# Kernel optimization log

Hardware: AMD Instinct MI355X
Metric: run time of the kernel (lower is better)

## Reference

```python
import jax, jax.numpy as jnp
import numpy as np

HEADS = 16
DIM_HEAD = 64


def setup_inputs() -> dict:
    key = jax.random.key(0)
    k1, k2, k3, k4 = jax.random.split(key, 4)
    B, T, D = 4, 1024, 1024
    x = jax.random.normal(k1, (B, T, D), dtype=jnp.float32)
    w_qkv = jax.random.normal(k2, (3 * HEADS * DIM_HEAD, D), dtype=jnp.float32) * (1.0 / np.sqrt(D))
    w_out = jax.random.normal(k3, (D, HEADS * DIM_HEAD), dtype=jnp.float32) * (1.0 / np.sqrt(HEADS * DIM_HEAD))
    rel_bias = jax.random.normal(k4, (2 * 1024 - 1, HEADS), dtype=jnp.float32) * 0.02
    return {"x": x, "w_qkv": w_qkv, "w_out": w_out, "rel_bias": rel_bias}


def reference(x, w_qkv, w_out, rel_bias):
    b, t, _ = x.shape
    h, dh = HEADS, DIM_HEAD
    scale = dh ** (-0.5)
    qkv = x @ w_qkv.T  # [b, t, 3*h*dh]
    # einops 'b t (d k h) -> k b h t d': last axis factors as (dh, 3, h)
    qkv = qkv.reshape(b, t, dh, 3, h).transpose(3, 0, 4, 1, 2)  # [3, b, h, t, dh]
    q, k, v = qkv[0], qkv[1], qkv[2]
    scores = jnp.einsum('bhid,bhjd->bhij', q, k) * scale  # [b, h, t, t]
    # relative position bias: rel[i,j] = j - i + t - 1
    rel = jnp.arange(t)[None, :] - jnp.arange(t)[:, None] + (t - 1)  # [t, t]
    bias = rel_bias[rel]  # [t, t, h]
    scores = scores + bias.transpose(2, 0, 1)[None]  # [b, h, t, t]
    attn = jax.nn.softmax(scores, axis=-1)
    out = jnp.einsum('bhij,bhjd->bhid', attn, v)  # [b, h, t, dh]
    out = out.transpose(0, 2, 1, 3).reshape(b, t, h * dh)  # 'b h t d -> b t (h d)'
    return out @ w_out.T
```

## Files before the change

### kernel.cpp

```cpp
#include <hip/hip_runtime.h>
#include <hip/hip_bf16.h>

typedef short bf16x8 __attribute__((ext_vector_type(8)));
typedef float f32x4  __attribute__((ext_vector_type(4)));

typedef __attribute__((address_space(3))) void lds_t;
typedef __attribute__((address_space(1))) void gbl_t;

#define MFMA16(a,b,c) __builtin_amdgcn_mfma_f32_16x16x32_bf16((a),(b),(c),0,0,0)

__device__ __forceinline__ unsigned short f2bf(float f) {
    __hip_bfloat16 h = __float2bfloat16(f);
    return __builtin_bit_cast(unsigned short, h);
}
__device__ __forceinline__ float bf2f(unsigned short u) {
    __hip_bfloat16 h = __builtin_bit_cast(__hip_bfloat16, u);
    return __bfloat162float(h);
}

__global__ void prep_all(const float* __restrict__ x,
                         const float* __restrict__ w_qkv,
                         const float* __restrict__ w_out,
                         unsigned short* __restrict__ A1h,
                         unsigned short* __restrict__ W1h,
                         unsigned short* __restrict__ W3h) {
    const int NX = 4096 * 256, NW1 = 3072 * 256, NW3 = 1024 * 256;
    for (int idx = blockIdx.x * blockDim.x + threadIdx.x; idx < NX + NW1 + NW3;
         idx += gridDim.x * blockDim.x) {
        if (idx < NX) {
            int base = idx * 4;
            float4 v = *reinterpret_cast<const float4*>(x + base);
            ushort4 hi;
            hi.x = f2bf(v.x); hi.y = f2bf(v.y);
            hi.z = f2bf(v.z); hi.w = f2bf(v.w);
            *reinterpret_cast<ushort4*>(A1h + base) = hi;
        } else if (idx < NX + NW1) {
            int base = (idx - NX) * 4;
            int n = base >> 10, c = base & 1023;
            int d = n & 63, which = n >> 10, h = (n >> 6) & 15;
            int srow = d * 48 + which * 16 + h;
            float4 v =
                *reinterpret_cast<const float4*>(w_qkv + (size_t)srow * 1024 + c);
            ushort4 hi;
            hi.x = f2bf(v.x); hi.y = f2bf(v.y);
            hi.z = f2bf(v.z); hi.w = f2bf(v.w);
            *reinterpret_cast<ushort4*>(W1h + (size_t)n * 1024 + c) = hi;
        } else {
            int base = (idx - NX - NW1) * 4;
            float4 v = *reinterpret_cast<const float4*>(w_out + base);
            ushort4 hi;
            hi.x = f2bf(v.x); hi.y = f2bf(v.y);
            hi.z = f2bf(v.z); hi.w = f2bf(v.w);
            *reinterpret_cast<ushort4*>(W3h + base) = hi;
        }
    }
}

__global__ __launch_bounds__(512, 2) void gemm256_hi(
    const unsigned short* __restrict__ A, const unsigned short* __restrict__ B,
    unsigned short* __restrict__ outQ, unsigned short* __restrict__ outK,
    unsigned short* __restrict__ outV) {
    __shared__ unsigned short lds[65536];
    const int tid = threadIdx.x;
    const int wid = tid >> 6, lane = tid & 63;
    const int lrow = lane & 15, lgrp = lane >> 4;
    const int wr = wid >> 2, wc = wid & 3;
    const int mtile = blockIdx.y * 256, ntile = blockIdx.x * 256;

    const int csw = lgrp ^ ((lrow >> 1) & 3);
    const int aoff = (wr * 128 + lrow) * 32 + csw * 8;
    const int boff = 32768 + (wc * 64 + lrow) * 32 + csw * 8;

    const int sreg = wid * 2;
    const int srow0 = sreg * 16 + (lane >> 2);
    const int srow1 = (sreg + 1) * 16 + (lane >> 2);
    const int schunk = (lane & 3) ^ ((lane >> 3) & 3);
    const int sdst0 = sreg * 512;

    f32x4 acc[8][4];
#pragma unroll
    for (int i = 0; i < 8; ++i)
#pragma unroll
        for (int j = 0; j < 4; ++j) {
            f32x4 z = {0.f, 0.f, 0.f, 0.f};
            acc[i][j] = z;
        }

#pragma unroll
    for (int s0 = 0; s0 < 2; ++s0) {
        const int kb = s0 * 32;
        __builtin_amdgcn_global_load_lds(
            (const gbl_t*)(A + (size_t)(mtile + srow0) * 1024 + kb + schunk * 8),
            (lds_t*)(lds + s0 * 8192 + sdst0), 16, 0, 0);
        __builtin_amdgcn_global_load_lds(
            (const gbl_t*)(A + (size_t)(mtile + srow1) * 1024 + kb + schunk * 8),
            (lds_t*)(lds + s0 * 8192 + sdst0 + 512), 16, 0, 0);
        __builtin_amdgcn_global_load_lds(
            (const gbl_t*)(B + (size_t)(ntile + srow0) * 1024 + kb + schunk * 8),
            (lds_t*)(lds + 32768 + s0 * 8192 + sdst0), 16, 0, 0);
        __builtin_amdgcn_global_load_lds(
            (const gbl_t*)(B + (size_t)(ntile + srow1) * 1024 + kb + schunk * 8),
            (lds_t*)(lds + 32768 + s0 * 8192 + sdst0 + 512), 16, 0, 0);
    }
    asm volatile("s_waitcnt vmcnt(4)" ::: "memory");
    __syncthreads();

    for (int s = 0; s < 32; ++s) {
        const int sa = s & 3;
        const unsigned short* sbase = lds + sa * 8192;

        bf16x8 af[8];
#pragma unroll
        for (int i = 0; i < 8; ++i)
            af[i] = *reinterpret_cast<const bf16x8*>(sbase + aoff + i * 512);
        bf16x8 b0 = *reinterpret_cast<const bf16x8*>(sbase + boff);
        bf16x8 b1 = *reinterpret_cast<const bf16x8*>(sbase + boff + 512);

        if (s <= 29) {
            const int kb2 = (s + 2) * 32;
            const int s2 = (s + 2) & 3;
            __builtin_amdgcn_global_load_lds(
                (const gbl_t*)(A + (size_t)(mtile + srow0) * 1024 + kb2 + schunk * 8),
                (lds_t*)(lds + s2 * 8192 + sdst0), 16, 0, 0);
            __builtin_amdgcn_global_load_lds(
                (const gbl_t*)(A + (size_t)(mtile + srow1) * 1024 + kb2 + schunk * 8),
                (lds_t*)(lds + s2 * 8192 + sdst0 + 512), 16, 0, 0);
        }
        __builtin_amdgcn_s_setprio(1);
#pragma unroll
        for (int i = 0; i < 8; ++i) {
            acc[i][0] = MFMA16(af[i], b0, acc[i][0]);
            acc[i][1] = MFMA16(af[i], b1, acc[i][1]);
        }
        __builtin_amdgcn_s_setprio(0);

        bf16x8 b2 = *reinterpret_cast<const bf16x8*>(sbase + boff + 1024);
        bf16x8 b3 = *reinterpret_cast<const bf16x8*>(sbase + boff + 1536);
        if (s <= 29) {
            const int kb2 = (s + 2) * 32;
            const int s2 = (s + 2) & 3;
            __builtin_amdgcn_global_load_lds(
                (const gbl_t*)(B + (size_t)(ntile + srow0) * 1024 + kb2 + schunk * 8),
                (lds_t*)(lds + 32768 + s2 * 8192 + sdst0), 16, 0, 0);
            __builtin_amdgcn_global_load_lds(
                (const gbl_t*)(B + (size_t)(ntile + srow1) * 1024 + kb2 + schunk * 8),
                (lds_t*)(lds + 32768 + s2 * 8192 + sdst0 + 512), 16, 0, 0);
        }
        __builtin_amdgcn_s_setprio(1);
#pragma unroll
        for (int i = 0; i < 8; ++i) {
            acc[i][2] = MFMA16(af[i], b2, acc[i][2]);
            acc[i][3] = MFMA16(af[i], b3, acc[i][3]);
        }
        __builtin_amdgcn_s_setprio(0);

        if (s < 31) {
            if (s <= 29)
                asm volatile("s_waitcnt vmcnt(4)" ::: "memory");
            else
                asm volatile("s_waitcnt vmcnt(0)" ::: "memory");
            __syncthreads();
        }
    }

#pragma unroll
    for (int i = 0; i < 8; ++i) {
#pragma unroll
        for (int j = 0; j < 4; ++j) {
#pragma unroll
            for (int r = 0; r < 4; ++r) {
                float v = acc[i][j][r];
                int m = mtile + wr * 128 + i * 16 + lgrp * 4 + r;
                int n = ntile + wc * 64 + j * 16 + lrow;
                int which = n >> 10;
                int hh = (n >> 6) & 15;
                int d = n & 63;
                int b = m >> 10, t = m & 1023;
                unsigned short* dstp =
                    (which == 0) ? outQ : ((which == 1) ? outK : outV);
                dstp[((size_t)((b << 4) + hh) * 1024 + t) * 64 + d] = f2bf(v);
            }
        }
    }
}

__global__ __launch_bounds__(256, 3) void gemm_out_v4(
    const unsigned short* __restrict__ A, const unsigned short* __restrict__ B,
    float* __restrict__ outF) {
    __shared__ unsigned short As[4][64 * 32];
    __shared__ unsigned short Bs[4][128 * 32];
    const int tid = threadIdx.x;
    const int wid = tid >> 6, lane = tid & 63;
    const int lrow = lane & 15, lgrp = lane >> 4;
    const int wr = wid >> 1, wc = wid & 1;
    const int h = blockIdx.x;
    const int xcd = h & 7, within = h >> 3;
    const int mtile = (xcd * 8 + (within & 7)) * 64;
    const int ntile = (within >> 3) * 128;

    const int csw = lgrp ^ ((lrow >> 1) & 3);
    const int aoff = (wr * 32 + lrow) * 32 + csw * 8;
    const int boff = (wc * 64 + lrow) * 32 + csw * 8;

    const int srow = tid >> 2;
    const int schunk = (tid & 3) ^ ((tid >> 3) & 3);
    const unsigned short* Arow = A + (size_t)(mtile + srow) * 1024 + schunk * 8;
    const unsigned short* Brow0 = B + (size_t)(ntile + srow) * 1024 + schunk * 8;
    const unsigned short* Brow1 =
        B + (size_t)(ntile + 64 + srow) * 1024 + schunk * 8;

    f32x4 acc[2][4];
#pragma unroll
    for (int i = 0; i < 2; ++i)
#pragma unroll
        for (int j = 0; j < 4; ++j) {
            f32x4 z = {0.f, 0.f, 0.f, 0.f};
            acc[i][j] = z;
        }

#pragma unroll
    for (int s0 = 0; s0 < 2; ++s0) {
        const int kb = s0 * 32;
        __builtin_amdgcn_global_load_lds((const gbl_t*)(Arow + kb),
                                         (lds_t*)(&As[s0][0] + tid * 8), 16, 0,
                                         0);
        __builtin_amdgcn_global_load_lds((const gbl_t*)(Brow0 + kb),
                                         (lds_t*)(&Bs[s0][0] + tid * 8), 16, 0,
                                         0);
        __builtin_amdgcn_global_load_lds((const gbl_t*)(Brow1 + kb),
                                         (lds_t*)(&Bs[s0][0] + 2048 + tid * 8),
                                         16, 0, 0);
    }
    asm volatile("s_waitcnt vmcnt(3)" ::: "memory");
    __syncthreads();

    for (int s = 0; s < 32; ++s) {
        const int sa = s & 3;
        if (s <= 29) {
            const int kb = (s + 2) * 32;
            const int s2 = (s + 2) & 3;
            __builtin_amdgcn_global_load_lds((const gbl_t*)(Arow + kb),
                                             (lds_t*)(&As[s2][0] + tid * 8), 16,
                                             0, 0);
            __builtin_amdgcn_global_load_lds((const gbl_t*)(Brow0 + kb),
                                             (lds_t*)(&Bs[s2][0] + tid * 8), 16,
                                             0, 0);
            __builtin_amdgcn_global_load_lds(
                (const gbl_t*)(Brow1 + kb),
                (lds_t*)(&Bs[s2][0] + 2048 + tid * 8), 16, 0, 0);
        }
        bf16x8 af[2], bfv[4];
#pragma unroll
        for (int i = 0; i < 2; ++i)
            af[i] = *reinterpret_cast<const bf16x8*>(&As[sa][0] + aoff + i * 512);
#pragma unroll
        for (int j = 0; j < 4; ++j)
            bfv[j] =
                *reinterpret_cast<const bf16x8*>(&Bs[sa][0] + boff + j * 512);
        __builtin_amdgcn_s_setprio(1);
#pragma unroll
        for (int i = 0; i < 2; ++i)
#pragma unroll
            for (int j = 0; j < 4; ++j)
                acc[i][j] = MFMA16(af[i], bfv[j], acc[i][j]);
        __builtin_amdgcn_s_setprio(0);
        if (s < 31) {
            if (s <= 29)
                asm volatile("s_waitcnt vmcnt(3)" ::: "memory");
            else
                asm volatile("s_waitcnt vmcnt(0)" ::: "memory");
            __syncthreads();
        }
    }

#pragma unroll
    for (int i = 0; i < 2; ++i)
#pragma unroll
        for (int j = 0; j < 4; ++j)
#pragma unroll
            for (int r = 0; r < 4; ++r) {
                int m = mtile + wr * 32 + i * 16 + lgrp * 4 + r;
                int n = ntile + wc * 64 + j * 16 + lrow;
                outF[(size_t)m * 1024 + n] = acc[i][j][r];
            }
}

__global__ __launch_bounds__(256) void transpose_v(
    const unsigned short* __restrict__ Vb, unsigned short* __restrict__ Vtg) {
    __shared__ unsigned short L[64][72];
    const int tt = blockIdx.x, bh = blockIdx.y;
    const int tid = threadIdx.x;
#pragma unroll
    for (int e = 0; e < 2; ++e) {
        int chunk = e * 256 + tid;
        int r = chunk >> 3, c = (chunk & 7) * 8;
        uint4 v = *reinterpret_cast<const uint4*>(
            Vb + ((size_t)bh * 1024 + tt * 64 + r) * 64 + c);
        *reinterpret_cast<uint4*>(&L[r][c]) = v;
    }
    __syncthreads();
#pragma unroll
    for (int e = 0; e < 2; ++e) {
        int chunk = e * 256 + tid;
        int d = chunk >> 3, t0 = (chunk & 7) * 8;
        unsigned short tmp[8];
#pragma unroll
        for (int u = 0; u < 8; ++u) tmp[u] = L[t0 + u][d];
        *reinterpret_cast<uint4*>(Vtg + ((size_t)bh * 64 + d) * 1024 + tt * 64 +
                                  t0) = *reinterpret_cast<const uint4*>(tmp);
    }
}

__global__ __launch_bounds__(512) void attn_kernel(
    const unsigned short* __restrict__ Qb, const unsigned short* __restrict__ Kb,
    const unsigned short* __restrict__ Vtg, const float* __restrict__ rel_bias,
    unsigned short* __restrict__ A3) {
    const int qt = blockIdx.x;
    const int bh = blockIdx.y;
    const int b = bh >> 4, h = bh & 15;
    const int tid = threadIdx.x;
    const int w = tid >> 6, lane = tid & 63;
    const int lrow = lane & 15, lgrp = lane >> 4;
    const float LOG2E = 1.4426950408889634f;
    const float SCALE2 = 0.125f * 1.4426950408889634f;
    const float THR = 11.5f;

    __shared__ unsigned short Ks[2][64 * 64];
    __shared__ unsigned short Vs[2][64 * 64];
    __shared__ unsigned short Ps[8][16 * 64];
    __shared__ float Bias2[2][192];

    const unsigned short* Ktile = Kb + (size_t)bh * 1024 * 64;
    const unsigned short* Vtile = Vtg + (size_t)bh * 64 * 1024;

    const unsigned short* Qp =
        Qb + ((size_t)bh * 1024 + qt * 128 + w * 16 + lrow) * 64;
    bf16x8 qa0 = *reinterpret_cast<const bf16x8*>(Qp + lgrp * 8);
    bf16x8 qa1 = *reinterpret_cast<const bf16x8*>(Qp + 32 + lgrp * 8);

    const int sr0 = w * 8 + (lane >> 3);
    const int sc_lo = lane & 7;

    float m_run = -3.0e38f;
    float l_run = 0.f;
    f32x4 o_acc[4];
#pragma unroll
    for (int n = 0; n < 4; n++) {
        f32x4 z = {0.f, 0.f, 0.f, 0.f};
        o_acc[n] = z;
    }

    const int bbase = lgrp * 4 + 127 - w * 16 - lrow;

    {
        {
            int r = sr0;
            int c = sc_lo ^ (r & 7);
            __builtin_amdgcn_global_load_lds(
                (const gbl_t*)(Ktile + (size_t)r * 64 + c * 8),
                (lds_t*)(&Ks[0][0] + w * 512), 16, 0, 0);
            __builtin_amdgcn_global_load_lds(
                (const gbl_t*)(Vtile + (size_t)r * 1024 + c * 8),
                (lds_t*)(&Vs[0][0] + w * 512), 16, 0, 0);
        }
        if (tid < 192) {
            int rowi = 0 - qt * 128 + 896 + tid;
            rowi = (rowi < 2046) ? rowi : 2046;
            Bias2[0][tid] = rel_bias[(size_t)rowi * 16 + h] * LOG2E;
        }
        asm volatile("s_waitcnt vmcnt(0)" ::: "memory");
        __syncthreads();
    }

    for (int kv = 0; kv < 16; ++kv) {
        const int cur = kv & 1;
        if (kv < 15) {
            const int j0n = (kv + 1) * 64;
            int r = sr0;
            int c = sc_lo ^ (r & 7);
            __builtin_amdgcn_global_load_lds(
                (const gbl_t*)(Ktile + (size_t)(j0n + r) * 64 + c * 8),
                (lds_t*)(&Ks[cur ^ 1][0] + w * 512), 16, 0, 0);
            __builtin_amdgcn_global_load_lds(
                (const gbl_t*)(Vtile + (size_t)r * 1024 + j0n + c * 8),
                (lds_t*)(&Vs[cur ^ 1][0] + w * 512), 16, 0, 0);
            if (tid < 192) {
                int rowi = j0n - qt * 128 + 896 + tid;
                rowi = (rowi < 2046) ? rowi : 2046;
                Bias2[cur ^ 1][tid] = rel_bias[(size_t)rowi * 16 + h] * LOG2E;
            }
        }

        const unsigned short* kbuf = &Ks[cur][0];
        f32x4 s[4];
        __builtin_amdgcn_s_setprio(1);
#pragma unroll
        for (int f = 0; f < 4; ++f) {
            int krow = f * 16 + lrow;
            int sw0 = (lgrp ^ (lrow & 7)) * 8;
            int sw1 = ((4 | lgrp) ^ (lrow & 7)) * 8;
            bf16x8 kb0 = *reinterpret_cast<const bf16x8*>(kbuf + krow * 64 + sw0);
            bf16x8 kb1 = *reinterpret_cast<const bf16x8*>(kbuf + krow * 64 + sw1);
            f32x4 z = {0.f, 0.f, 0.f, 0.f};
            z = MFMA16(kb0, qa0, z);
            z = MFMA16(kb1, qa1, z);
            s[f] = z;
        }
        __builtin_amdgcn_s_setprio(0);

        float x[4][4];
        float pm = -3.0e38f;
#pragma unroll
        for (int f = 0; f < 4; ++f)
#pragma unroll
            for (int r = 0; r < 4; ++r) {
                float xv = s[f][r] * SCALE2 + Bias2[cur][bbase + f * 16 + r];
                x[f][r] = xv;
                pm = fmaxf(pm, xv);
            }
        pm = fmaxf(pm, __shfl_xor(pm, 16));
        pm = fmaxf(pm, __shfl_xor(pm, 32));

        if (!__all(pm - m_run <= THR)) {
            float mnew = fmaxf(m_run, pm);
            float corr = __builtin_amdgcn_exp2f(m_run - mnew);
            m_run = mnew;
            l_run *= corr;
            float cb[4];
#pragma unroll
            for (int r = 0; r < 4; ++r) cb[r] = __shfl(corr, lgrp * 4 + r);
#pragma unroll
            for (int n = 0; n < 4; n++)
#pragma unroll
                for (int r = 0; r < 4; r++) o_acc[n][r] *= cb[r];
        }

        float su = 0.f;
#pragma unroll
        for (int f = 0; f < 4; ++f)
#pragma unroll
            for (int r = 0; r < 4; ++r) {
                float pv = __builtin_amdgcn_exp2f(x[f][r] - m_run);
                x[f][r] = pv;
                su += pv;
            }
        l_run += su;

#pragma unroll
        for (int f = 0; f < 4; ++f) {
            unsigned int plo, phi;
            asm("v_cvt_pk_bf16_f32 %0, %1, %2"
                : "=v"(plo)
                : "v"(x[f][0]), "v"(x[f][1]));
            asm("v_cvt_pk_bf16_f32 %0, %1, %2"
                : "=v"(phi)
                : "v"(x[f][2]), "v"(x[f][3]));
            const int chunk = (f * 2 + (lgrp >> 1)) ^ (lrow & 7);
            uint2 pw;
            pw.x = plo;
            pw.y = phi;
            *reinterpret_cast<uint2*>(
                &Ps[w][lrow * 64 + chunk * 8 + (lgrp & 1) * 4]) = pw;
        }

        const unsigned short* vbuf = &Vs[cur][0];
        __builtin_amdgcn_s_setprio(1);
#pragma unroll
        for (int jc = 0; jc < 2; ++jc) {
            int pc = ((4 * jc + lgrp) ^ (lrow & 7)) * 8;
            bf16x8 pa =
                *reinterpret_cast<const bf16x8*>(&Ps[w][0] + lrow * 64 + pc);
#pragma unroll
            for (int n = 0; n < 4; n++) {
                int vrow = n * 16 + lrow;
                bf16x8 vb =
                    *reinterpret_cast<const bf16x8*>(vbuf + vrow * 64 + pc);
                o_acc[n] = MFMA16(pa, vb, o_acc[n]);
            }
        }
        __builtin_amdgcn_s_setprio(0);

        if (kv < 15) {
            asm volatile("s_waitcnt vmcnt(0)" ::: "memory");
            __syncthreads();
        }
    }

    float lt = l_run + __shfl_xor(l_run, 16);
    lt += __shfl_xor(lt, 32);
    float rl[4];
#pragma unroll
    for (int r = 0; r < 4; ++r) rl[r] = 1.0f / __shfl(lt, lgrp * 4 + r);

#pragma unroll
    for (int n = 0; n < 4; n++) {
#pragma unroll
        for (int r = 0; r < 4; r++) {
            float val = o_acc[n][r] * rl[r];
            int ia = qt * 128 + w * 16 + lgrp * 4 + r;
            size_t m = (size_t)b * 1024 + ia;
            int col = h * 64 + n * 16 + lrow;
            A3[m * 1024 + col] = f2bf(val);
        }
    }
}

extern "C" void kernel_launch(void* const* d_in, const int* in_sizes, int n_in,
                              void* d_out, int out_size, void* d_ws,
                              size_t ws_size, hipStream_t stream) {
    const float* x = (const float*)d_in[0];
    const float* w_qkv = (const float*)d_in[1];
    const float* w_out = (const float*)d_in[2];
    const float* rel_bias = (const float*)d_in[3];
    float* out = (float*)d_out;

    char* ws = (char*)d_ws;
    size_t off = 0;
    auto alloc = [&](size_t bytes) {
        char* p = ws + off;
        off += (bytes + 255) & ~(size_t)255;
        return p;
    };
    unsigned short* A1h = (unsigned short*)alloc((size_t)4096 * 1024 * 2);
    unsigned short* W1h = (unsigned short*)alloc((size_t)3072 * 1024 * 2);
    unsigned short* Qb = (unsigned short*)alloc((size_t)64 * 1024 * 64 * 2);
    unsigned short* Kb = (unsigned short*)alloc((size_t)64 * 1024 * 64 * 2);
    unsigned short* Vb = (unsigned short*)alloc((size_t)64 * 1024 * 64 * 2);
    unsigned short* A3h = (unsigned short*)alloc((size_t)4096 * 1024 * 2);
    unsigned short* W3h = (unsigned short*)alloc((size_t)1024 * 1024 * 2);
    unsigned short* Vtg = A1h;

    hipLaunchKernelGGL(prep_all, dim3(2048), dim3(256), 0, stream, x, w_qkv,
                       w_out, A1h, W1h, W3h);
    hipLaunchKernelGGL(gemm256_hi, dim3(12, 16), dim3(512), 0, stream, A1h, W1h,
                       Qb, Kb, Vb);
    hipLaunchKernelGGL(transpose_v, dim3(16, 64), dim3(256), 0, stream, Vb, Vtg);
    hipLaunchKernelGGL(attn_kernel, dim3(8, 64), dim3(512), 0, stream, Qb, Kb,
                       Vtg, rel_bias, A3h);
    hipLaunchKernelGGL(gemm_out_v4, dim3(512), dim3(256), 0, stream, A3h, W3h,
                       out);
}
```

Measured before the change: 108.6 us.

## Use 64-wide K double-buffered tiles in out-proj GEMM and preload full bias row

The output projection GEMM moves from a four-stage ring of 32-wide K slices to two buffers of 64-wide K slices. This halves the number of loop iterations and barriers, and its XOR swizzle now spans eight 16-byte chunks. The attention kernel loads the whole relative-bias window for the query tile into LDS once, so the per-iteration bias loads and their double-buffer slot are gone. The cost is a shallower prefetch in the GEMM, since each step now waits for vmcnt(0), and a larger bias LDS footprint that can reduce occupancy.

```diff
diff --git a/kernel.cpp b/kernel.cpp
--- a/kernel.cpp
+++ b/kernel.cpp
@@ -184,11 +184,11 @@
     }
 }
 
-__global__ __launch_bounds__(256, 3) void gemm_out_v4(
+__global__ __launch_bounds__(256, 3) void gemm_out_v5(
     const unsigned short* __restrict__ A, const unsigned short* __restrict__ B,
     float* __restrict__ outF) {
-    __shared__ unsigned short As[4][64 * 32];
-    __shared__ unsigned short Bs[4][128 * 32];
+    __shared__ unsigned short As[2][64 * 64];
+    __shared__ unsigned short Bs[2][128 * 64];
     const int tid = threadIdx.x;
     const int wid = tid >> 6, lane = tid & 63;
     const int lrow = lane & 15, lgrp = lane >> 4;
@@ -198,16 +198,15 @@
     const int mtile = (xcd * 8 + (within & 7)) * 64;
     const int ntile = (within >> 3) * 128;
 
-    const int csw = lgrp ^ ((lrow >> 1) & 3);
-    const int aoff = (wr * 32 + lrow) * 32 + csw * 8;
-    const int boff = (wc * 64 + lrow) * 32 + csw * 8;
-
-    const int srow = tid >> 2;
-    const int schunk = (tid & 3) ^ ((tid >> 3) & 3);
-    const unsigned short* Arow = A + (size_t)(mtile + srow) * 1024 + schunk * 8;
-    const unsigned short* Brow0 = B + (size_t)(ntile + srow) * 1024 + schunk * 8;
-    const unsigned short* Brow1 =
-        B + (size_t)(ntile + 64 + srow) * 1024 + schunk * 8;
+    const int srow = tid >> 3;
+    const int schunk = (tid & 7) ^ (srow & 7);
+    const unsigned short* Abase = A + (size_t)(mtile + srow) * 1024 + schunk * 8;
+    const unsigned short* Bbase = B + (size_t)(ntile + srow) * 1024 + schunk * 8;
+
+    const int csw0 = (lgrp ^ (lrow & 7)) * 8;
+    const int csw1 = ((4 | lgrp) ^ (lrow & 7)) * 8;
+    const int arow = wr * 32 + lrow;
+    const int brow = wc * 64 + lrow;
 
     f32x4 acc[2][4];
 #pragma unroll
@@ -219,56 +218,60 @@
         }
 
 #pragma unroll
-    for (int s0 = 0; s0 < 2; ++s0) {
-        const int kb = s0 * 32;
-        __builtin_amdgcn_global_load_lds((const gbl_t*)(Arow + kb),
-                                         (lds_t*)(&As[s0][0] + tid * 8), 16, 0,
-                                         0);
-        __builtin_amdgcn_global_load_lds((const gbl_t*)(Brow0 + kb),
-                                         (lds_t*)(&Bs[s0][0] + tid * 8), 16, 0,
-                                         0);
-        __builtin_amdgcn_global_load_lds((const gbl_t*)(Brow1 + kb),
-                                         (lds_t*)(&Bs[s0][0] + 2048 + tid * 8),
-                                         16, 0, 0);
-    }
-    asm volatile("s_waitcnt vmcnt(3)" ::: "memory");
+    for (int e = 0; e < 2; ++e)
+        __builtin_amdgcn_global_load_lds(
+            (const gbl_t*)(Abase + (size_t)e * 32 * 1024),
+            (lds_t*)(&As[0][0] + e * 2048 + tid * 8), 16, 0, 0);
+#pragma unroll
+    for (int e = 0; e < 4; ++e)
+        __builtin_amdgcn_global_load_lds(
+            (const gbl_t*)(Bbase + (size_t)e * 32 * 1024),
+            (lds_t*)(&Bs[0][0] + e * 2048 + tid * 8), 16, 0, 0);
+    asm volatile("s_waitcnt vmcnt(0)" ::: "memory");
     __syncthreads();
 
-    for (int s = 0; s < 32; ++s) {
-        const int sa = s & 3;
-        if (s <= 29) {
-            const int kb = (s + 2) * 32;
-            const int s2 = (s + 2) & 3;
-            __builtin_amdgcn_global_load_lds((const gbl_t*)(Arow + kb),
-                                             (lds_t*)(&As[s2][0] + tid * 8), 16,
-                                             0, 0);
-            __builtin_amdgcn_global_load_lds((const gbl_t*)(Brow0 + kb),
-                                             (lds_t*)(&Bs[s2][0] + tid * 8), 16,
-                                             0, 0);
-            __builtin_amdgcn_global_load_lds(
-                (const gbl_t*)(Brow1 + kb),
-                (lds_t*)(&Bs[s2][0] + 2048 + tid * 8), 16, 0, 0);
-        }
-        bf16x8 af[2], bfv[4];
+    for (int s = 0; s < 16; ++s) {
+        const int cur = s & 1;
+        if (s < 15) {
+            const int kb = (s + 1) * 64;
+            const int nx = cur ^ 1;
+#pragma unroll
+            for (int e = 0; e < 2; ++e)
+                __builtin_amdgcn_global_load_lds(
+                    (const gbl_t*)(Abase + (size_t)e * 32 * 1024 + kb),
+                    (lds_t*)(&As[nx][0] + e * 2048 + tid * 8), 16, 0, 0);
+#pragma unroll
+            for (int e = 0; e < 4; ++e)
+                __builtin_amdgcn_global_load_lds(
+                    (const gbl_t*)(Bbase + (size_t)e * 32 * 1024 + kb),
+                    (lds_t*)(&Bs[nx][0] + e * 2048 + tid * 8), 16, 0, 0);
+        }
+        bf16x8 a0[2], a1[2], b0[4], b1[4];
+#pragma unroll
+        for (int i = 0; i < 2; ++i) {
+            a0[i] = *reinterpret_cast<const bf16x8*>(&As[cur][0] +
+                                                     (arow + i * 16) * 64 + csw0);
+            a1[i] = *reinterpret_cast<const bf16x8*>(&As[cur][0] +
+                                                     (arow + i * 16) * 64 + csw1);
+        }
+#pragma unroll
+        for (int j = 0; j < 4; ++j) {
+            b0[j] = *reinterpret_cast<const bf16x8*>(&Bs[cur][0] +
+                                                     (brow + j * 16) * 64 + csw0);
+            b1[j] = *reinterpret_cast<const bf16x8*>(&Bs[cur][0] +
+                                                     (brow + j * 16) * 64 + csw1);
+        }
+        __builtin_amdgcn_s_setprio(1);
 #pragma unroll
         for (int i = 0; i < 2; ++i)
-            af[i] = *reinterpret_cast<const bf16x8*>(&As[sa][0] + aoff + i * 512);
-#pragma unroll
-        for (int j = 0; j < 4; ++j)
-            bfv[j] =
-                *reinterpret_cast<const bf16x8*>(&Bs[sa][0] + boff + j * 512);
-        __builtin_amdgcn_s_setprio(1);
-#pragma unroll
-        for (int i = 0; i < 2; ++i)
-#pragma unroll
-            for (int j = 0; j < 4; ++j)
-                acc[i][j] = MFMA16(af[i], bfv[j], acc[i][j]);
+#pragma unroll
+            for (int j = 0; j < 4; ++j) {
+                acc[i][j] = MFMA16(a0[i], b0[j], acc[i][j]);
+                acc[i][j] = MFMA16(a1[i], b1[j], acc[i][j]);
+            }
         __builtin_amdgcn_s_setprio(0);
-        if (s < 31) {
-            if (s <= 29)
-                asm volatile("s_waitcnt vmcnt(3)" ::: "memory");
-            else
-                asm volatile("s_waitcnt vmcnt(0)" ::: "memory");
+        if (s < 15) {
+            asm volatile("s_waitcnt vmcnt(0)" ::: "memory");
             __syncthreads();
         }
     }
@@ -328,7 +331,7 @@
     __shared__ unsigned short Ks[2][64 * 64];
     __shared__ unsigned short Vs[2][64 * 64];
     __shared__ unsigned short Ps[8][16 * 64];
-    __shared__ float Bias2[2][192];
+    __shared__ float BiasF[1152];
 
     const unsigned short* Ktile = Kb + (size_t)bh * 1024 * 64;
     const unsigned short* Vtile = Vtg + (size_t)bh * 64 * 1024;
@@ -363,17 +366,16 @@
                 (const gbl_t*)(Vtile + (size_t)r * 1024 + c * 8),
                 (lds_t*)(&Vs[0][0] + w * 512), 16, 0, 0);
         }
-        if (tid < 192) {
-            int rowi = 0 - qt * 128 + 896 + tid;
-            rowi = (rowi < 2046) ? rowi : 2046;
-            Bias2[0][tid] = rel_bias[(size_t)rowi * 16 + h] * LOG2E;
-        }
+        const int rbase = 896 - qt * 128;
+        for (int t = tid; t < 1151; t += 512)
+            BiasF[t] = rel_bias[(size_t)(t + rbase) * 16 + h] * LOG2E;
         asm volatile("s_waitcnt vmcnt(0)" ::: "memory");
         __syncthreads();
     }
 
     for (int kv = 0; kv < 16; ++kv) {
         const int cur = kv & 1;
+        const int j0 = kv * 64;
         if (kv < 15) {
             const int j0n = (kv + 1) * 64;
             int r = sr0;
@@ -384,11 +386,6 @@
             __builtin_amdgcn_global_load_lds(
                 (const gbl_t*)(Vtile + (size_t)r * 1024 + j0n + c * 8),
                 (lds_t*)(&Vs[cur ^ 1][0] + w * 512), 16, 0, 0);
-            if (tid < 192) {
-                int rowi = j0n - qt * 128 + 896 + tid;
-                rowi = (rowi < 2046) ? rowi : 2046;
-                Bias2[cur ^ 1][tid] = rel_bias[(size_t)rowi * 16 + h] * LOG2E;
-            }
         }
 
         const unsigned short* kbuf = &Ks[cur][0];
@@ -414,7 +411,7 @@
         for (int f = 0; f < 4; ++f)
 #pragma unroll
             for (int r = 0; r < 4; ++r) {
-                float xv = s[f][r] * SCALE2 + Bias2[cur][bbase + f * 16 + r];
+                float xv = s[f][r] * SCALE2 + BiasF[j0 + bbase + f * 16 + r];
                 x[f][r] = xv;
                 pm = fmaxf(pm, xv);
             }
@@ -537,6 +534,6 @@
     hipLaunchKernelGGL(transpose_v, dim3(16, 64), dim3(256), 0, stream, Vb, Vtg);
     hipLaunchKernelGGL(attn_kernel, dim3(8, 64), dim3(512), 0, stream, Qb, Kb,
                        Vtg, rel_bias, A3h);
-    hipLaunchKernelGGL(gemm_out_v4, dim3(512), dim3(256), 0, stream, A3h, W3h,
+    hipLaunchKernelGGL(gemm_out_v5, dim3(512), dim3(256), 0, stream, A3h, W3h,
                        out);
 }
```

After: 105.2 us. -3.1%, faster.
